# Kernel tuning notes

Measured on AMD Instinct MI355X. Metric: run time of the kernel, lower is better.

Reference implementation:

```python
import jax, jax.numpy as jnp
import numpy as np

DIM = 192
HEADS = 6
WS = (4, 4, 4)
N = 64          # prod(WS)
NW = 64         # windows per sample
BATCH = 2048    # num_windows * B
CPB_HIDDEN = 512


def _make_rpb_tables():
    space = len(WS)
    coords = [np.arange(-(w - 1), w, dtype=np.float32) for w in WS]
    rpb = np.stack(np.meshgrid(*coords, indexing='ij'))  # (3, 7,7,7)
    for i in range(space):
        rpb[i] = rpb[i] / (WS[i] - 1)
    rpb = np.moveaxis(rpb, 0, -1)[None]  # (1,7,7,7,3)
    rpb = 8.0 * rpb
    rpb = np.sign(rpb) * np.log2(np.abs(rpb) + 1.0) / np.log2(8.0)
    grid = np.stack(np.meshgrid(*[np.arange(w) for w in WS], indexing='ij')).reshape(space, -1)  # (3, N)
    dists = grid[:, :, None] - grid[:, None, :]  # (3, N, N)
    for i in range(space):
        center = max(int(np.prod([2 * w - 1 for w in WS[i + 1:]])), 1)
        dists[i] = (dists[i] + WS[i] - 1) * center
    rpb_idx = dists.sum(0)  # (N, N), values in [0, 343)
    return jnp.asarray(rpb, jnp.float32), jnp.asarray(rpb_idx, jnp.int32)


def setup_inputs() -> dict:
    key = jax.random.key(0)
    ks = jax.random.split(key, 8)
    rpb, rpb_idx = _make_rpb_tables()
    s = 0.02
    return {
        'x': jax.random.normal(ks[0], (BATCH, N, DIM), jnp.float32),
        'mask': jnp.zeros((NW, N, N), jnp.float32),
        'rpb': rpb,
        'rpb_idx': rpb_idx,
        'cpb_w1': jax.random.normal(ks[1], (CPB_HIDDEN, len(WS)), jnp.float32) * s,
        'cpb_b1': jnp.zeros((CPB_HIDDEN,), jnp.float32),
        'cpb_w2': jax.random.normal(ks[2], (HEADS, CPB_HIDDEN), jnp.float32) * s,
        'qkv_w': jax.random.normal(ks[3], (3 * DIM, DIM), jnp.float32) * s,
        'qkv_b': jnp.zeros((3 * DIM,), jnp.float32),
        'proj_w': jax.random.normal(ks[4], (DIM, DIM), jnp.float32) * s,
        'proj_b': jnp.zeros((DIM,), jnp.float32),
        'logit_scale': jnp.log(10.0 * jnp.ones((HEADS, 1, 1), jnp.float32)),
    }


def reference(x, mask, rpb, rpb_idx, cpb_w1, cpb_b1, cpb_w2, qkv_w, qkv_b,
              proj_w, proj_b, logit_scale):
    B, n, C = x.shape
    H = logit_scale.shape[0]
    hd = C // H
    # qkv projection -> (3, B, H, n, hd)
    qkv = (x @ qkv_w.T + qkv_b).reshape(B, n, 3, H, hd).transpose(2, 0, 3, 1, 4)
    q, k, v = qkv[0], qkv[1], qkv[2]
    # continuous position bias MLP: (1,7,7,7,3) -> (1,7,7,7,H) -> gather -> (1,H,n,n)
    h1 = jax.nn.relu(rpb @ cpb_w1.T + cpb_b1)
    bias = (h1 @ cpb_w2.T).reshape(-1, H)            # (343, H)
    bias = bias[rpb_idx.reshape(-1)].reshape(n, n, H)
    bias = 16.0 * jax.nn.sigmoid(bias)
    bias = bias.transpose(2, 0, 1)[None]             # (1, H, n, n)
    # cosine attention
    qn = q / jnp.maximum(jnp.linalg.norm(q, axis=-1, keepdims=True), 1e-12)
    kn = k / jnp.maximum(jnp.linalg.norm(k, axis=-1, keepdims=True), 1e-12)
    scale = jnp.exp(jnp.minimum(logit_scale, jnp.log(jnp.float32(100.0))))  # clamp max=log(1/0.01)
    attn = jnp.einsum('bhnd,bhmd->bhnm', qn, kn) * scale + bias
    nW = mask.shape[0]
    attn = attn + jnp.tile(mask[:, None, :, :], (B // nW, 1, 1, 1))  # (B,1,n,n) broadcast over heads
    attn = jax.nn.softmax(attn, axis=-1)
    out = jnp.einsum('bhnm,bhmd->bhnd', attn, v)
    out = out.transpose(0, 2, 1, 3).reshape(B, n, C)  # heads-major concat (b n (h c))
    return out @ proj_w.T + proj_b
```

## Files before the change

kernel.cpp:

```cpp
#include <hip/hip_runtime.h>
#include <hip/hip_bf16.h>

#define DIM 192
#define HEADS 6
#define HD 32
#define NTOK 64
#define BATCH 2048
#define CPBH 512
#define TBL 343
#define NW 64

typedef unsigned int u32;
typedef __attribute__((ext_vector_type(8))) short b16x8;
typedef __attribute__((ext_vector_type(4))) float f32x4;

__device__ __forceinline__ unsigned short f2bf(float f) {
  union { __hip_bfloat16 h; unsigned short s; } cv;
  cv.h = __float2bfloat16(f);
  return cv.s;
}
__device__ __forceinline__ u32 pack2(float a, float b) {
  return (u32)f2bf(a) | ((u32)f2bf(b) << 16);
}
union FragU { u32 u[4]; b16x8 s; uint4 q; };

__device__ __forceinline__ b16x8 ld_frag_g(const u32* p) {
  FragU f; f.q = *(const uint4*)p; return f.s;
}

__global__ __launch_bounds__(64) void k_cpb1(
    const float* __restrict__ rpb, const float* __restrict__ w1,
    const float* __restrict__ b1, const float* __restrict__ w2,
    float* __restrict__ tab) {
  int t = blockIdx.x, lane = threadIdx.x;
  float r0 = rpb[t*3], r1 = rpb[t*3+1], r2 = rpb[t*3+2];
  float a[HEADS];
  #pragma unroll
  for (int h = 0; h < HEADS; ++h) a[h] = 0.f;
  #pragma unroll
  for (int kk = 0; kk < 8; ++kk) {
    int k = lane * 8 + kk;
    float hv = fmaf(r0, w1[k*3], fmaf(r1, w1[k*3+1], fmaf(r2, w1[k*3+2], b1[k])));
    hv = fmaxf(hv, 0.f);
    #pragma unroll
    for (int h = 0; h < HEADS; ++h) a[h] = fmaf(hv, w2[h*CPBH + k], a[h]);
  }
  #pragma unroll
  for (int h = 0; h < HEADS; ++h) {
    a[h] += __shfl_xor(a[h], 1);  a[h] += __shfl_xor(a[h], 2);
    a[h] += __shfl_xor(a[h], 4);  a[h] += __shfl_xor(a[h], 8);
    a[h] += __shfl_xor(a[h], 16); a[h] += __shfl_xor(a[h], 32);
  }
  if (lane == 0) {
    #pragma unroll
    for (int h = 0; h < HEADS; ++h) tab[t*HEADS + h] = a[h];
  }
}

__global__ void k_bm(const float* __restrict__ tab, const int* __restrict__ ridx,
                     const float* __restrict__ mask, float* __restrict__ bm) {
  int idx = blockIdx.x * blockDim.x + threadIdx.x;
  if (idx >= NW * HEADS * 4096) return;
  int ij = idx & 4095;
  int h = (idx >> 12) % HEADS;
  int nw = idx / (HEADS * 4096);
  float v = tab[ridx[ij] * HEADS + h];
  bm[idx] = 16.f / (1.f + __expf(-v)) + mask[nw * 4096 + ij];
}

__global__ void k_wcvt(const float* __restrict__ qkvw, const float* __restrict__ pw,
                       u32* __restrict__ wq, u32* __restrict__ wp) {
  int i = blockIdx.x * blockDim.x + threadIdx.x;
  if (i < 55296) {
    wq[i] = pack2(qkvw[2*i], qkvw[2*i+1]);
  } else if (i < 55296 + 18432) {
    int j = i - 55296;
    wp[j] = pack2(pw[2*j], pw[2*j+1]);
  }
}

__global__ __launch_bounds__(384) void k_qkv(
    const float* __restrict__ x, const u32* __restrict__ wq,
    const float* __restrict__ bias,
    u32* __restrict__ qo, u32* __restrict__ ko, u32* __restrict__ vT) {
  __shared__ u32 xl[NTOK * 101];
  const int tid = threadIdx.x;
  const int b = blockIdx.x;
  const float4* xg = (const float4*)(x + (size_t)b * (NTOK * DIM));
  for (int i = tid; i < (NTOK * DIM) / 4; i += 384) {
    float4 v = xg[i];
    int flat = i * 4, tok = flat / DIM, k = flat % DIM;
    xl[tok*101 + k/2]     = pack2(v.x, v.y);
    xl[tok*101 + k/2 + 1] = pack2(v.z, v.w);
  }
  __syncthreads();
  const int lane = tid & 63;
  const int wv = tid >> 6;
  const int m = lane & 15;
  const int qd = lane >> 4;
  const int sel = wv >> 1;
  u32* dst = (sel == 0) ? qo : (sel == 1) ? ko : vT;
  #pragma unroll 1
  for (int p = 0; p < 3; ++p) {
    const int h = (wv & 1) * 3 + p;
    const int jbase = wv * 96 + p * 32;
    b16x8 afr[2][6];
    float bv[2][4];
    #pragma unroll
    for (int half = 0; half < 2; ++half) {
      const u32* wp = wq + (size_t)(jbase + half*16 + m) * 96;
      #pragma unroll
      for (int ks = 0; ks < 6; ++ks) afr[half][ks] = ld_frag_g(wp + ks*16 + qd*4);
      #pragma unroll
      for (int r = 0; r < 4; ++r) bv[half][r] = bias[jbase + half*16 + qd*4 + r];
    }
    const size_t bh1024 = ((size_t)b * HEADS + h) * 1024;
    #pragma unroll 1
    for (int tp = 0; tp < 2; ++tp) {
      f32x4 acc[2][2];
      #pragma unroll
      for (int tt = 0; tt < 2; ++tt) {
        acc[tt][0] = (f32x4){0.f,0.f,0.f,0.f};
        acc[tt][1] = (f32x4){0.f,0.f,0.f,0.f};
      }
      #pragma unroll
      for (int ks = 0; ks < 6; ++ks) {
        #pragma unroll
        for (int tt = 0; tt < 2; ++tt) {
          b16x8 bfr = *(const b16x8*)(&xl[((tp*2+tt)*16 + m)*101 + ks*16 + qd*4]);
          acc[tt][0] = __builtin_amdgcn_mfma_f32_16x16x32_bf16(afr[0][ks], bfr, acc[tt][0], 0,0,0);
          acc[tt][1] = __builtin_amdgcn_mfma_f32_16x16x32_bf16(afr[1][ks], bfr, acc[tt][1], 0,0,0);
        }
      }
      #pragma unroll
      for (int tt = 0; tt < 2; ++tt) {
        const int t = tp*2 + tt;
        f32x4 acc0 = acc[tt][0], acc1 = acc[tt][1];
        #pragma unroll
        for (int r = 0; r < 4; ++r) { acc0[r] += bv[0][r]; acc1[r] += bv[1][r]; }
        if (sel < 2) {
          float ss = 0.f;
          #pragma unroll
          for (int r = 0; r < 4; ++r) ss = fmaf(acc0[r],acc0[r], fmaf(acc1[r],acc1[r], ss));
          ss += __shfl_xor(ss, 16);
          ss += __shfl_xor(ss, 32);
          float inv = 1.f / fmaxf(sqrtf(ss), 1e-12f);
          #pragma unroll
          for (int r = 0; r < 4; ++r) { acc0[r] *= inv; acc1[r] *= inv; }
          int tok = t*16 + m;
          u32* o = dst + bh1024 + tok*16;
          *(uint2*)(o + qd*2)     = make_uint2(pack2(acc0[0],acc0[1]), pack2(acc0[2],acc0[3]));
          *(uint2*)(o + 8 + qd*2) = make_uint2(pack2(acc1[0],acc1[1]), pack2(acc1[2],acc1[3]));
        } else {
          float p0[8];
          #pragma unroll
          for (int r = 0; r < 4; ++r) { p0[r] = acc0[r]; p0[4+r] = acc1[r]; }
          float pr[8];
          #pragma unroll
          for (int e = 0; e < 8; ++e) pr[e] = __shfl_xor(p0[e], 1);
          if ((m & 1) == 0) {
            #pragma unroll
            for (int e = 0; e < 8; ++e) {
              int d = (e >> 2)*16 + qd*4 + (e & 3);
              dst[bh1024 + d*32 + (t*16 + m)/2] = pack2(p0[e], pr[e]);
            }
          }
        }
      }
    }
  }
}

__global__ __launch_bounds__(384) void k_attn_proj(
    const u32* __restrict__ qo, const u32* __restrict__ ko, const u32* __restrict__ vT,
    const float* __restrict__ bm, const float* __restrict__ ls,
    const u32* __restrict__ wp, const float* __restrict__ pb,
    float* __restrict__ out) {
  __shared__ u32 pbuf[HEADS][64 * 35];
  __shared__ u32 aol[64 * 99];
  const int tid = threadIdx.x;
  const int b = blockIdx.x;
  const int h = tid >> 6;
  const int lane = tid & 63;
  const int m = lane & 15, qd = lane >> 4;
  const size_t bh1024 = ((size_t)b * HEADS + h) * 1024;

  b16x8 qfr[4], kfr[4];
  #pragma unroll
  for (int mt = 0; mt < 4; ++mt) qfr[mt] = ld_frag_g(qo + bh1024 + (mt*16 + m)*16 + qd*4);
  #pragma unroll
  for (int ct = 0; ct < 4; ++ct) kfr[ct] = ld_frag_g(ko + bh1024 + (ct*16 + m)*16 + qd*4);

  f32x4 s[4][4];
  #pragma unroll
  for (int mt = 0; mt < 4; ++mt)
    #pragma unroll
    for (int ct = 0; ct < 4; ++ct) {
      f32x4 z = {0.f,0.f,0.f,0.f};
      s[mt][ct] = __builtin_amdgcn_mfma_f32_16x16x32_bf16(qfr[mt], kfr[ct], z, 0,0,0);
    }

  const float sc = __expf(fminf(ls[h], 4.60517019f));
  const float* bmp = bm + ((size_t)(b & 63) * HEADS + h) * 4096;
  #pragma unroll
  for (int mt = 0; mt < 4; ++mt)
    #pragma unroll
    for (int ct = 0; ct < 4; ++ct) {
      #pragma unroll
      for (int r = 0; r < 4; ++r) {
        int row = mt*16 + qd*4 + r, col = ct*16 + m;
        s[mt][ct][r] = fmaf(s[mt][ct][r], sc, bmp[row*64 + col]);
      }
    }
  float rinv[4][4];
  u32* pbw = pbuf[h];
  #pragma unroll
  for (int mt = 0; mt < 4; ++mt) {
    #pragma unroll
    for (int r = 0; r < 4; ++r) {
      float mm = s[mt][0][r];
      #pragma unroll
      for (int ct = 1; ct < 4; ++ct) mm = fmaxf(mm, s[mt][ct][r]);
      mm = fmaxf(mm, __shfl_xor(mm, 1)); mm = fmaxf(mm, __shfl_xor(mm, 2));
      mm = fmaxf(mm, __shfl_xor(mm, 4)); mm = fmaxf(mm, __shfl_xor(mm, 8));
      float l = 0.f;
      #pragma unroll
      for (int ct = 0; ct < 4; ++ct) { s[mt][ct][r] = __expf(s[mt][ct][r] - mm); l += s[mt][ct][r]; }
      l += __shfl_xor(l, 1); l += __shfl_xor(l, 2);
      l += __shfl_xor(l, 4); l += __shfl_xor(l, 8);
      rinv[mt][r] = 1.f / l;
      int row = mt*16 + qd*4 + r;
      #pragma unroll
      for (int ct = 0; ct < 4; ++ct) {
        float pv = s[mt][ct][r];
        float pn = __shfl_xor(pv, 1);
        if ((m & 1) == 0) pbw[row*35 + ct*8 + (m >> 1)] = pack2(pv, pn);
      }
    }
  }
  b16x8 vfr[2][2];
  #pragma unroll
  for (int nt = 0; nt < 2; ++nt)
    #pragma unroll
    for (int ks = 0; ks < 2; ++ks)
      vfr[nt][ks] = ld_frag_g(vT + bh1024 + (nt*16 + m)*32 + ks*16 + qd*4);
  #pragma unroll
  for (int mt = 0; mt < 4; ++mt) {
    b16x8 pa0 = *(const b16x8*)(&pbw[(mt*16 + m)*35 + qd*4]);
    b16x8 pa1 = *(const b16x8*)(&pbw[(mt*16 + m)*35 + 16 + qd*4]);
    #pragma unroll
    for (int nt = 0; nt < 2; ++nt) {
      f32x4 o = {0.f,0.f,0.f,0.f};
      o = __builtin_amdgcn_mfma_f32_16x16x32_bf16(pa0, vfr[nt][0], o, 0,0,0);
      o = __builtin_amdgcn_mfma_f32_16x16x32_bf16(pa1, vfr[nt][1], o, 0,0,0);
      #pragma unroll
      for (int r = 0; r < 4; ++r) {
        float val = o[r] * rinv[mt][r];
        float pn = __shfl_xor(val, 1);
        if ((m & 1) == 0) {
          int row = mt*16 + qd*4 + r;
          aol[row*99 + h*16 + nt*8 + (m >> 1)] = pack2(val, pn);
        }
      }
    }
  }
  __syncthreads();
  const int wv = h;
  b16x8 afr[2][6];
  float bv[2][4];
  #pragma unroll
  for (int jj = 0; jj < 2; ++jj) {
    const u32* wrow = wp + (size_t)((wv*2 + jj)*16 + m) * 96;
    #pragma unroll
    for (int ks = 0; ks < 6; ++ks) afr[jj][ks] = ld_frag_g(wrow + ks*16 + qd*4);
    #pragma unroll
    for (int r = 0; r < 4; ++r) bv[jj][r] = pb[(wv*2 + jj)*16 + qd*4 + r];
  }
  #pragma unroll 1
  for (int t = 0; t < 4; ++t) {
    f32x4 acc0 = {0.f,0.f,0.f,0.f}, acc1 = {0.f,0.f,0.f,0.f};
    #pragma unroll
    for (int ks = 0; ks < 6; ++ks) {
      b16x8 bfr = *(const b16x8*)(&aol[(t*16 + m)*99 + ks*16 + qd*4]);
      acc0 = __builtin_amdgcn_mfma_f32_16x16x32_bf16(afr[0][ks], bfr, acc0, 0,0,0);
      acc1 = __builtin_amdgcn_mfma_f32_16x16x32_bf16(afr[1][ks], bfr, acc1, 0,0,0);
    }
    float* op = out + ((size_t)b*64 + t*16 + m) * DIM;
    *(float4*)(op + (wv*2+0)*16 + qd*4) =
        make_float4(acc0[0]+bv[0][0], acc0[1]+bv[0][1], acc0[2]+bv[0][2], acc0[3]+bv[0][3]);
    *(float4*)(op + (wv*2+1)*16 + qd*4) =
        make_float4(acc1[0]+bv[1][0], acc1[1]+bv[1][1], acc1[2]+bv[1][2], acc1[3]+bv[1][3]);
  }
}

extern "C" void kernel_launch(void* const* d_in, const int* in_sizes, int n_in,
                              void* d_out, int out_size, void* d_ws, size_t ws_size,
                              hipStream_t stream) {
  const float* x    = (const float*)d_in[0];
  const float* mask = (const float*)d_in[1];
  const float* rpb  = (const float*)d_in[2];
  const int*   ridx = (const int*)d_in[3];
  const float* w1   = (const float*)d_in[4];
  const float* b1   = (const float*)d_in[5];
  const float* w2   = (const float*)d_in[6];
  const float* qkvw = (const float*)d_in[7];
  const float* qkvb = (const float*)d_in[8];
  const float* pw   = (const float*)d_in[9];
  const float* pb   = (const float*)d_in[10];
  const float* ls   = (const float*)d_in[11];
  float* out = (float*)d_out;

  char* ws = (char*)d_ws;
  const size_t QS = (size_t)BATCH * HEADS * NTOK * HD * 2;
  u32* qo = (u32*)(ws);
  u32* ko = (u32*)(ws + QS);
  u32* vT = (u32*)(ws + 2 * QS);
  float* btab = (float*)(ws + 3 * QS);
  float* bm   = (float*)(ws + 3 * QS + 16384);
  u32* wq = (u32*)(ws + 3 * QS + 16384 + 6291456);
  u32* wp = (u32*)(ws + 3 * QS + 16384 + 6291456 + 221184);

  k_cpb1<<<TBL, 64, 0, stream>>>(rpb, w1, b1, w2, btab);
  k_wcvt<<<(73728 + 255) / 256, 256, 0, stream>>>(qkvw, pw, wq, wp);
  k_bm<<<(NW * HEADS * 4096 + 255) / 256, 256, 0, stream>>>(btab, ridx, mask, bm);
  k_qkv<<<BATCH, 384, 0, stream>>>(x, wq, qkvb, qo, ko, vT);
  k_attn_proj<<<BATCH, 384, 0, stream>>>(qo, ko, vT, bm, ls, wp, pb, out);
}
```

Before: 418.4 us.

## Fuse QKV projection into attention kernel, keep Q/K/V on-chip

Merges the QKV projection and attention+proj kernels into one kernel per window. Each wave computes its own head's Q, K, V; Q and K stay in registers as MFMA fragments and V goes to LDS transposed. The QKV weights are permuted at conversion time so the accumulator layout matches the fragment layout. This removes the global write and read of the bf16 Q/K/V intermediates and one launch, at the cost of more registers and LDS per block (launch bounds set to 3 blocks per CU).

```diff
diff --git a/kernel.cpp b/kernel.cpp
--- a/kernel.cpp
+++ b/kernel.cpp
@@ -72,182 +72,151 @@
                        u32* __restrict__ wq, u32* __restrict__ wp) {
   int i = blockIdx.x * blockDim.x + threadIdx.x;
   if (i < 55296) {
-    wq[i] = pack2(qkvw[2*i], qkvw[2*i+1]);
+    int R = i / 96, c = i % 96;
+    int h  = R / 96;
+    int t  = R - h * 96;
+    int s3 = t >> 5;
+    int u  = t & 31;
+    int hf = (u >> 4) & 1;
+    int p  = u & 15;
+    int d  = ((p >> 2) << 3) + (hf << 2) + (p & 3);
+    int orig = s3 * 192 + h * 32 + d;
+    wq[i] = pack2(qkvw[orig*192 + 2*c], qkvw[orig*192 + 2*c + 1]);
   } else if (i < 55296 + 18432) {
     int j = i - 55296;
     wp[j] = pack2(pw[2*j], pw[2*j+1]);
   }
 }
 
-__global__ __launch_bounds__(384) void k_qkv(
+__global__ __launch_bounds__(384, 3) void k_fused(
     const float* __restrict__ x, const u32* __restrict__ wq,
-    const float* __restrict__ bias,
-    u32* __restrict__ qo, u32* __restrict__ ko, u32* __restrict__ vT) {
-  __shared__ u32 xl[NTOK * 101];
-  const int tid = threadIdx.x;
-  const int b = blockIdx.x;
-  const float4* xg = (const float4*)(x + (size_t)b * (NTOK * DIM));
-  for (int i = tid; i < (NTOK * DIM) / 4; i += 384) {
-    float4 v = xg[i];
-    int flat = i * 4, tok = flat / DIM, k = flat % DIM;
-    xl[tok*101 + k/2]     = pack2(v.x, v.y);
-    xl[tok*101 + k/2 + 1] = pack2(v.z, v.w);
-  }
-  __syncthreads();
-  const int lane = tid & 63;
-  const int wv = tid >> 6;
-  const int m = lane & 15;
-  const int qd = lane >> 4;
-  const int sel = wv >> 1;
-  u32* dst = (sel == 0) ? qo : (sel == 1) ? ko : vT;
-  #pragma unroll 1
-  for (int p = 0; p < 3; ++p) {
-    const int h = (wv & 1) * 3 + p;
-    const int jbase = wv * 96 + p * 32;
-    b16x8 afr[2][6];
-    float bv[2][4];
-    #pragma unroll
-    for (int half = 0; half < 2; ++half) {
-      const u32* wp = wq + (size_t)(jbase + half*16 + m) * 96;
-      #pragma unroll
-      for (int ks = 0; ks < 6; ++ks) afr[half][ks] = ld_frag_g(wp + ks*16 + qd*4);
-      #pragma unroll
-      for (int r = 0; r < 4; ++r) bv[half][r] = bias[jbase + half*16 + qd*4 + r];
-    }
-    const size_t bh1024 = ((size_t)b * HEADS + h) * 1024;
-    #pragma unroll 1
-    for (int tp = 0; tp < 2; ++tp) {
-      f32x4 acc[2][2];
-      #pragma unroll
-      for (int tt = 0; tt < 2; ++tt) {
-        acc[tt][0] = (f32x4){0.f,0.f,0.f,0.f};
-        acc[tt][1] = (f32x4){0.f,0.f,0.f,0.f};
-      }
-      #pragma unroll
-      for (int ks = 0; ks < 6; ++ks) {
-        #pragma unroll
-        for (int tt = 0; tt < 2; ++tt) {
-          b16x8 bfr = *(const b16x8*)(&xl[((tp*2+tt)*16 + m)*101 + ks*16 + qd*4]);
-          acc[tt][0] = __builtin_amdgcn_mfma_f32_16x16x32_bf16(afr[0][ks], bfr, acc[tt][0], 0,0,0);
-          acc[tt][1] = __builtin_amdgcn_mfma_f32_16x16x32_bf16(afr[1][ks], bfr, acc[tt][1], 0,0,0);
-        }
-      }
-      #pragma unroll
-      for (int tt = 0; tt < 2; ++tt) {
-        const int t = tp*2 + tt;
-        f32x4 acc0 = acc[tt][0], acc1 = acc[tt][1];
-        #pragma unroll
-        for (int r = 0; r < 4; ++r) { acc0[r] += bv[0][r]; acc1[r] += bv[1][r]; }
-        if (sel < 2) {
-          float ss = 0.f;
-          #pragma unroll
-          for (int r = 0; r < 4; ++r) ss = fmaf(acc0[r],acc0[r], fmaf(acc1[r],acc1[r], ss));
-          ss += __shfl_xor(ss, 16);
-          ss += __shfl_xor(ss, 32);
-          float inv = 1.f / fmaxf(sqrtf(ss), 1e-12f);
-          #pragma unroll
-          for (int r = 0; r < 4; ++r) { acc0[r] *= inv; acc1[r] *= inv; }
-          int tok = t*16 + m;
-          u32* o = dst + bh1024 + tok*16;
-          *(uint2*)(o + qd*2)     = make_uint2(pack2(acc0[0],acc0[1]), pack2(acc0[2],acc0[3]));
-          *(uint2*)(o + 8 + qd*2) = make_uint2(pack2(acc1[0],acc1[1]), pack2(acc1[2],acc1[3]));
-        } else {
-          float p0[8];
-          #pragma unroll
-          for (int r = 0; r < 4; ++r) { p0[r] = acc0[r]; p0[4+r] = acc1[r]; }
-          float pr[8];
-          #pragma unroll
-          for (int e = 0; e < 8; ++e) pr[e] = __shfl_xor(p0[e], 1);
-          if ((m & 1) == 0) {
-            #pragma unroll
-            for (int e = 0; e < 8; ++e) {
-              int d = (e >> 2)*16 + qd*4 + (e & 3);
-              dst[bh1024 + d*32 + (t*16 + m)/2] = pack2(p0[e], pr[e]);
-            }
-          }
-        }
-      }
-    }
-  }
-}
-
-__global__ __launch_bounds__(384) void k_attn_proj(
-    const u32* __restrict__ qo, const u32* __restrict__ ko, const u32* __restrict__ vT,
-    const float* __restrict__ bm, const float* __restrict__ ls,
-    const u32* __restrict__ wp, const float* __restrict__ pb,
-    float* __restrict__ out) {
-  __shared__ u32 pbuf[HEADS][64 * 35];
-  __shared__ u32 aol[64 * 99];
+    const float* __restrict__ qkvb, const float* __restrict__ bm,
+    const float* __restrict__ ls, const u32* __restrict__ wp,
+    const float* __restrict__ pb, float* __restrict__ out) {
+  union ShU { u32 xl[NTOK * 101]; u32 aol[NTOK * 99]; };
+  __shared__ ShU un;
+  __shared__ u32 vTL[HEADS][32 * 35];
+  __shared__ u32 pbt[HEADS][16 * 35];
+
   const int tid = threadIdx.x;
   const int b = blockIdx.x;
   const int h = tid >> 6;
   const int lane = tid & 63;
   const int m = lane & 15, qd = lane >> 4;
-  const size_t bh1024 = ((size_t)b * HEADS + h) * 1024;
-
-  b16x8 qfr[4], kfr[4];
-  #pragma unroll
-  for (int mt = 0; mt < 4; ++mt) qfr[mt] = ld_frag_g(qo + bh1024 + (mt*16 + m)*16 + qd*4);
-  #pragma unroll
-  for (int ct = 0; ct < 4; ++ct) kfr[ct] = ld_frag_g(ko + bh1024 + (ct*16 + m)*16 + qd*4);
-
-  f32x4 s[4][4];
-  #pragma unroll
-  for (int mt = 0; mt < 4; ++mt)
+
+  {
+    const float4* xg = (const float4*)(x + (size_t)b * (NTOK * DIM));
+    for (int i = tid; i < (NTOK * DIM) / 4; i += 384) {
+      float4 v = xg[i];
+      int flat = i * 4, tok = flat / DIM, k = flat % DIM;
+      un.xl[tok*101 + k/2]     = pack2(v.x, v.y);
+      un.xl[tok*101 + k/2 + 1] = pack2(v.z, v.w);
+    }
+  }
+  __syncthreads();
+
+  b16x8 qfv[4], kfv[4];
+  #pragma unroll
+  for (int s3 = 0; s3 < 3; ++s3) {
+    b16x8 afr[2][6];
+    float bv[2][4];
+    #pragma unroll
+    for (int hf = 0; hf < 2; ++hf) {
+      const u32* wrow = wq + (size_t)(((h*3 + s3)*2 + hf)*16 + m) * 96;
+      #pragma unroll
+      for (int ks = 0; ks < 6; ++ks) afr[hf][ks] = ld_frag_g(wrow + ks*16 + qd*4);
+      #pragma unroll
+      for (int r = 0; r < 4; ++r) bv[hf][r] = qkvb[s3*192 + h*32 + qd*8 + hf*4 + r];
+    }
+    #pragma unroll
+    for (int t = 0; t < 4; ++t) {
+      f32x4 a0 = {0.f,0.f,0.f,0.f}, a1 = {0.f,0.f,0.f,0.f};
+      #pragma unroll
+      for (int ks = 0; ks < 6; ++ks) {
+        b16x8 bfr = *(const b16x8*)(&un.xl[(t*16 + m)*101 + ks*16 + qd*4]);
+        a0 = __builtin_amdgcn_mfma_f32_16x16x32_bf16(afr[0][ks], bfr, a0, 0,0,0);
+        a1 = __builtin_amdgcn_mfma_f32_16x16x32_bf16(afr[1][ks], bfr, a1, 0,0,0);
+      }
+      #pragma unroll
+      for (int r = 0; r < 4; ++r) { a0[r] += bv[0][r]; a1[r] += bv[1][r]; }
+      if (s3 < 2) {
+        float ss = 0.f;
+        #pragma unroll
+        for (int r = 0; r < 4; ++r) ss = fmaf(a0[r],a0[r], fmaf(a1[r],a1[r], ss));
+        ss += __shfl_xor(ss, 16);
+        ss += __shfl_xor(ss, 32);
+        float inv = 1.f / fmaxf(sqrtf(ss), 1e-12f);
+        FragU tf;
+        tf.u[0] = pack2(a0[0]*inv, a0[1]*inv);
+        tf.u[1] = pack2(a0[2]*inv, a0[3]*inv);
+        tf.u[2] = pack2(a1[0]*inv, a1[1]*inv);
+        tf.u[3] = pack2(a1[2]*inv, a1[3]*inv);
+        if (s3 == 0) qfv[t] = tf.s; else kfv[t] = tf.s;
+      } else {
+        float v8[8];
+        #pragma unroll
+        for (int r = 0; r < 4; ++r) { v8[r] = a0[r]; v8[4+r] = a1[r]; }
+        #pragma unroll
+        for (int e = 0; e < 8; ++e) {
+          float pn = __shfl_xor(v8[e], 1);
+          if ((m & 1) == 0) {
+            int d = qd*8 + (e>>2)*4 + (e&3);
+            vTL[h][d*35 + t*8 + (m>>1)] = pack2(v8[e], pn);
+          }
+        }
+      }
+    }
+  }
+  __syncthreads();
+
+  const float sc = __expf(fminf(ls[h], 4.60517019f));
+  const float* bmp = bm + ((size_t)(b & 63) * HEADS + h) * 4096;
+  b16x8 vfr[2][2];
+  #pragma unroll
+  for (int nt = 0; nt < 2; ++nt)
+    #pragma unroll
+    for (int ks = 0; ks < 2; ++ks)
+      vfr[nt][ks] = *(const b16x8*)(&vTL[h][(nt*16 + m)*35 + ks*16 + qd*4]);
+  u32* pbw = pbt[h];
+  #pragma unroll
+  for (int mt = 0; mt < 4; ++mt) {
+    f32x4 s4[4];
     #pragma unroll
     for (int ct = 0; ct < 4; ++ct) {
       f32x4 z = {0.f,0.f,0.f,0.f};
-      s[mt][ct] = __builtin_amdgcn_mfma_f32_16x16x32_bf16(qfr[mt], kfr[ct], z, 0,0,0);
-    }
-
-  const float sc = __expf(fminf(ls[h], 4.60517019f));
-  const float* bmp = bm + ((size_t)(b & 63) * HEADS + h) * 4096;
-  #pragma unroll
-  for (int mt = 0; mt < 4; ++mt)
-    #pragma unroll
-    for (int ct = 0; ct < 4; ++ct) {
+      s4[ct] = __builtin_amdgcn_mfma_f32_16x16x32_bf16(qfv[mt], kfv[ct], z, 0,0,0);
+    }
+    #pragma unroll
+    for (int ct = 0; ct < 4; ++ct)
       #pragma unroll
       for (int r = 0; r < 4; ++r) {
         int row = mt*16 + qd*4 + r, col = ct*16 + m;
-        s[mt][ct][r] = fmaf(s[mt][ct][r], sc, bmp[row*64 + col]);
-      }
-    }
-  float rinv[4][4];
-  u32* pbw = pbuf[h];
-  #pragma unroll
-  for (int mt = 0; mt < 4; ++mt) {
+        s4[ct][r] = fmaf(s4[ct][r], sc, bmp[row*64 + col]);
+      }
+    float rinv[4];
     #pragma unroll
     for (int r = 0; r < 4; ++r) {
-      float mm = s[mt][0][r];
-      #pragma unroll
-      for (int ct = 1; ct < 4; ++ct) mm = fmaxf(mm, s[mt][ct][r]);
+      float mm = s4[0][r];
+      #pragma unroll
+      for (int ct = 1; ct < 4; ++ct) mm = fmaxf(mm, s4[ct][r]);
       mm = fmaxf(mm, __shfl_xor(mm, 1)); mm = fmaxf(mm, __shfl_xor(mm, 2));
       mm = fmaxf(mm, __shfl_xor(mm, 4)); mm = fmaxf(mm, __shfl_xor(mm, 8));
       float l = 0.f;
       #pragma unroll
-      for (int ct = 0; ct < 4; ++ct) { s[mt][ct][r] = __expf(s[mt][ct][r] - mm); l += s[mt][ct][r]; }
+      for (int ct = 0; ct < 4; ++ct) { s4[ct][r] = __expf(s4[ct][r] - mm); l += s4[ct][r]; }
       l += __shfl_xor(l, 1); l += __shfl_xor(l, 2);
       l += __shfl_xor(l, 4); l += __shfl_xor(l, 8);
-      rinv[mt][r] = 1.f / l;
-      int row = mt*16 + qd*4 + r;
+      rinv[r] = 1.f / l;
+      int rloc = qd*4 + r;
       #pragma unroll
       for (int ct = 0; ct < 4; ++ct) {
-        float pv = s[mt][ct][r];
+        float pv = s4[ct][r];
         float pn = __shfl_xor(pv, 1);
-        if ((m & 1) == 0) pbw[row*35 + ct*8 + (m >> 1)] = pack2(pv, pn);
-      }
-    }
-  }
-  b16x8 vfr[2][2];
-  #pragma unroll
-  for (int nt = 0; nt < 2; ++nt)
-    #pragma unroll
-    for (int ks = 0; ks < 2; ++ks)
-      vfr[nt][ks] = ld_frag_g(vT + bh1024 + (nt*16 + m)*32 + ks*16 + qd*4);
-  #pragma unroll
-  for (int mt = 0; mt < 4; ++mt) {
-    b16x8 pa0 = *(const b16x8*)(&pbw[(mt*16 + m)*35 + qd*4]);
-    b16x8 pa1 = *(const b16x8*)(&pbw[(mt*16 + m)*35 + 16 + qd*4]);
+        if ((m & 1) == 0) pbw[rloc*35 + ct*8 + (m >> 1)] = pack2(pv, pn);
+      }
+    }
+    b16x8 pa0 = *(const b16x8*)(&pbw[m*35 + qd*4]);
+    b16x8 pa1 = *(const b16x8*)(&pbw[m*35 + 16 + qd*4]);
     #pragma unroll
     for (int nt = 0; nt < 2; ++nt) {
       f32x4 o = {0.f,0.f,0.f,0.f};
@@ -255,41 +224,40 @@
       o = __builtin_amdgcn_mfma_f32_16x16x32_bf16(pa1, vfr[nt][1], o, 0,0,0);
       #pragma unroll
       for (int r = 0; r < 4; ++r) {
-        float val = o[r] * rinv[mt][r];
+        float val = o[r] * rinv[r];
         float pn = __shfl_xor(val, 1);
-        if ((m & 1) == 0) {
-          int row = mt*16 + qd*4 + r;
-          aol[row*99 + h*16 + nt*8 + (m >> 1)] = pack2(val, pn);
-        }
+        if ((m & 1) == 0)
+          un.aol[(mt*16 + qd*4 + r)*99 + h*16 + nt*8 + (m >> 1)] = pack2(val, pn);
       }
     }
   }
   __syncthreads();
+
   const int wv = h;
-  b16x8 afr[2][6];
-  float bv[2][4];
+  b16x8 pfr[2][6];
+  float pbv[2][4];
   #pragma unroll
   for (int jj = 0; jj < 2; ++jj) {
     const u32* wrow = wp + (size_t)((wv*2 + jj)*16 + m) * 96;
     #pragma unroll
-    for (int ks = 0; ks < 6; ++ks) afr[jj][ks] = ld_frag_g(wrow + ks*16 + qd*4);
-    #pragma unroll
-    for (int r = 0; r < 4; ++r) bv[jj][r] = pb[(wv*2 + jj)*16 + qd*4 + r];
+    for (int ks = 0; ks < 6; ++ks) pfr[jj][ks] = ld_frag_g(wrow + ks*16 + qd*4);
+    #pragma unroll
+    for (int r = 0; r < 4; ++r) pbv[jj][r] = pb[(wv*2 + jj)*16 + qd*4 + r];
   }
   #pragma unroll 1
   for (int t = 0; t < 4; ++t) {
     f32x4 acc0 = {0.f,0.f,0.f,0.f}, acc1 = {0.f,0.f,0.f,0.f};
     #pragma unroll
     for (int ks = 0; ks < 6; ++ks) {
-      b16x8 bfr = *(const b16x8*)(&aol[(t*16 + m)*99 + ks*16 + qd*4]);
-      acc0 = __builtin_amdgcn_mfma_f32_16x16x32_bf16(afr[0][ks], bfr, acc0, 0,0,0);
-      acc1 = __builtin_amdgcn_mfma_f32_16x16x32_bf16(afr[1][ks], bfr, acc1, 0,0,0);
+      b16x8 bfr = *(const b16x8*)(&un.aol[(t*16 + m)*99 + ks*16 + qd*4]);
+      acc0 = __builtin_amdgcn_mfma_f32_16x16x32_bf16(pfr[0][ks], bfr, acc0, 0,0,0);
+      acc1 = __builtin_amdgcn_mfma_f32_16x16x32_bf16(pfr[1][ks], bfr, acc1, 0,0,0);
     }
     float* op = out + ((size_t)b*64 + t*16 + m) * DIM;
     *(float4*)(op + (wv*2+0)*16 + qd*4) =
-        make_float4(acc0[0]+bv[0][0], acc0[1]+bv[0][1], acc0[2]+bv[0][2], acc0[3]+bv[0][3]);
+        make_float4(acc0[0]+pbv[0][0], acc0[1]+pbv[0][1], acc0[2]+pbv[0][2], acc0[3]+pbv[0][3]);
     *(float4*)(op + (wv*2+1)*16 + qd*4) =
-        make_float4(acc1[0]+bv[1][0], acc1[1]+bv[1][1], acc1[2]+bv[1][2], acc1[3]+bv[1][3]);
+        make_float4(acc1[0]+pbv[1][0], acc1[1]+pbv[1][1], acc1[2]+pbv[1][2], acc1[3]+pbv[1][3]);
   }
 }
 
@@ -311,18 +279,13 @@
   float* out = (float*)d_out;
 
   char* ws = (char*)d_ws;
-  const size_t QS = (size_t)BATCH * HEADS * NTOK * HD * 2;
-  u32* qo = (u32*)(ws);
-  u32* ko = (u32*)(ws + QS);
-  u32* vT = (u32*)(ws + 2 * QS);
-  float* btab = (float*)(ws + 3 * QS);
-  float* bm   = (float*)(ws + 3 * QS + 16384);
-  u32* wq = (u32*)(ws + 3 * QS + 16384 + 6291456);
-  u32* wp = (u32*)(ws + 3 * QS + 16384 + 6291456 + 221184);
+  float* btab = (float*)(ws);
+  float* bm   = (float*)(ws + 16384);
+  u32* wq = (u32*)(ws + 16384 + 6291456);
+  u32* wp = (u32*)(ws + 16384 + 6291456 + 221184);
 
   k_cpb1<<<TBL, 64, 0, stream>>>(rpb, w1, b1, w2, btab);
   k_wcvt<<<(73728 + 255) / 256, 256, 0, stream>>>(qkvw, pw, wq, wp);
   k_bm<<<(NW * HEADS * 4096 + 255) / 256, 256, 0, stream>>>(btab, ridx, mask, bm);
-  k_qkv<<<BATCH, 384, 0, stream>>>(x, wq, qkvb, qo, ko, vT);
-  k_attn_proj<<<BATCH, 384, 0, stream>>>(qo, ko, vT, bm, ls, wp, pb, out);
-}
+  k_fused<<<BATCH, 384, 0, stream>>>(x, wq, qkvb, bm, ls, wp, pb, out);
+}
```

After: 447.9 us. 1.07x slower.
